# Kernel optimization log

Measured on AMD Instinct MI355X. Metric: run time of the kernel, lower is better.

## Reference

```python
import jax, jax.numpy as jnp
import numpy as np

EPS = 1e-5  # BatchNorm eps (eval mode, running mean 0 / var 1)
NEG_SLOPE = 0.2


def _knn_idx(x, k):
    # x: [B,C,N] -> idx [B,N,k] (indices of k largest of negative sq dist = k nearest)
    inner = jnp.einsum('bcn,bcm->bnm', x, x)
    xx = jnp.sum(x * x, axis=1)  # [B,N]
    pd = 2.0 * inner - xx[:, :, None] - xx[:, None, :]
    return jax.lax.top_k(pd, k)[1]


def _edge_feature(x, k):
    # x: [B,C,N] -> edge features [B,2C,N,k] = concat(neighbor - center, center)
    idx = _knn_idx(x, k)                        # [B,N,k]
    xt = jnp.transpose(x, (0, 2, 1))            # [B,N,C]
    nbr = jax.vmap(lambda f, i: f[i])(xt, idx)  # [B,N,k,C] gather per batch
    ctr = jnp.broadcast_to(xt[:, :, None, :], nbr.shape)
    feat = jnp.concatenate([nbr - ctr, ctr], axis=-1)  # [B,N,k,2C]
    return jnp.transpose(feat, (0, 3, 1, 2))


def _bn(x, g, b):
    # eval-mode BatchNorm: running_mean=0, running_var=1 -> x * g/sqrt(1+eps) + b
    inv = 1.0 / np.sqrt(1.0 + EPS)
    sh = (1, -1) + (1,) * (x.ndim - 2)
    return x * (g * inv).reshape(sh) + b.reshape(sh)


def _lrelu(x):
    return jnp.where(x >= 0, x, NEG_SLOPE * x)


def _conv2d(x, w, b):  # 1x1 Conv2d: x [B,Ci,N,K], w [Ci,Co]
    return jnp.einsum('bcnk,co->bonk', x, w) + b[None, :, None, None]


def _conv1d(x, w, b):  # 1x1 Conv1d: x [B,Ci,N], w [Ci,Co]
    return jnp.einsum('bcn,co->bon', x, w) + b[None, :, None]


def setup_inputs() -> dict:
    key = jax.random.key(0)
    ks = jax.random.split(key, 24)
    B, N = 8, 4096
    rn = lambda k, sh, s=0.1: (jax.random.normal(k, sh, dtype=jnp.float32) * s)
    inp = {
        'point': jax.random.normal(ks[0], (B, 3, N), dtype=jnp.float32),
        # conv1_1: Conv2d(6,64)
        'w11': rn(ks[1], (6, 64)), 'b11': rn(ks[2], (64,)),
        'g11': jnp.ones((64,), jnp.float32), 'bb11': jnp.zeros((64,), jnp.float32),
        # conv1_2: Conv2d(6,64)
        'w12': rn(ks[3], (6, 64)), 'b12': rn(ks[4], (64,)),
        'g12': jnp.ones((64,), jnp.float32), 'bb12': jnp.zeros((64,), jnp.float32),
        # conv1_3: Conv1d(128,64)
        'w13': rn(ks[5], (128, 64)), 'b13': rn(ks[6], (64,)),
        'g13': jnp.ones((64,), jnp.float32), 'bb13': jnp.zeros((64,), jnp.float32),
        # conv1_5: Conv2d(128,64)
        'w15': rn(ks[7], (128, 64)), 'b15': rn(ks[8], (64,)),
        'g15': jnp.ones((64,), jnp.float32), 'bb15': jnp.zeros((64,), jnp.float32),
        # conv1_4: Conv1d(64,128)
        'w14': rn(ks[9], (64, 128)), 'b14': rn(ks[10], (128,)),
        'g14': jnp.ones((128,), jnp.float32), 'bb14': jnp.zeros((128,), jnp.float32),
        # fc1: Linear(128,64) + ReLU + Linear(64,3)
        'wf1': rn(ks[11], (128, 64)), 'bf1': rn(ks[12], (64,)),
        'wf2': rn(ks[13], (64, 3)), 'bf2': rn(ks[14], (3,)),
    }
    return inp


def reference(point, w11, b11, g11, bb11, w12, b12, g12, bb12,
              w13, b13, g13, bb13, w15, b15, g15, bb15,
              w14, b14, g14, bb14, wf1, bf1, wf2, bf2):
    # point: [B,3,N]
    f = _edge_feature(point, 8)                    # [B,6,N,8]
    f1 = _lrelu(_bn(_conv2d(f, w11, b11), g11, bb11)).max(axis=-1)   # [B,64,N]
    f = _edge_feature(point, 16)                   # [B,6,N,16]
    f2 = _lrelu(_bn(_conv2d(f, w12, b12), g12, bb12)).max(axis=-1)   # [B,64,N]
    f = jnp.concatenate([f1, f2], axis=1)          # [B,128,N]
    f = _lrelu(_bn(_conv1d(f, w13, b13), g13, bb13))                 # [B,64,N]
    g = _edge_feature(f, 16)                       # [B,128,N,16]
    g = _lrelu(_bn(_conv2d(g, w15, b15), g15, bb15)).max(axis=-1)    # [B,64,N]
    g = _lrelu(_bn(_conv1d(g, w14, b14), g14, bb14))                 # [B,128,N]
    feat = jnp.transpose(g, (0, 2, 1))             # [B,N,128]
    h = jax.nn.relu(feat @ wf1 + bf1) @ wf2 + bf2  # [B,N,3]
    refinepoint = h + jnp.transpose(point, (0, 2, 1))
    return feat, refinepoint
```

## Files before the change

kernel.cpp:

```cpp
#include <hip/hip_runtime.h>
#include <math.h>

#define NB 8
#define NP 4096
#define FEAT_SZ (NB * NP * 128)
#define INVBN 0.9999950000374999f
#define SPLIT 2
#define CHUNKS 32

typedef unsigned long long u64;
typedef unsigned int u32;

__device__ __forceinline__ u32 fmap(float f) {
    u32 b = __float_as_uint(f);
    return b ^ ((u32)((int)b >> 31) | 0x80000000u);
}

__device__ __forceinline__ u64 umax64(u64 a, u64 b) { return a > b ? a : b; }

__device__ __forceinline__ void kins(u64 (&v)[16], u64 key) {
    if (key <= v[15]) return;
    bool bb[16];
#pragma unroll
    for (int j = 0; j < 16; ++j) bb[j] = key > v[j];
#pragma unroll
    for (int j = 15; j >= 1; --j) v[j] = bb[j] ? (bb[j - 1] ? v[j - 1] : key) : v[j];
    if (bb[0]) v[0] = key;
}

__device__ __forceinline__ void bufpush(u64 (&v)[16], u64 &q0, u64 &q1, u64 &q2, u64 &q3,
                                        int &cnt, u64 key) {
    if (cnt < 4) {
        q0 = cnt == 0 ? key : q0;
        q1 = cnt == 1 ? key : q1;
        q2 = cnt == 2 ? key : q2;
        q3 = cnt == 3 ? key : q3;
        ++cnt;
    } else {
        kins(v, key);
    }
}

__device__ __forceinline__ void bufflush(u64 (&v)[16], u64 &q0, u64 &q1, u64 &q2, u64 &q3,
                                         int &cnt) {
    kins(v, q0); kins(v, q1); kins(v, q2); kins(v, q3);
    q0 = 0; q1 = 0; q2 = 0; q3 = 0; cnt = 0;
}

__device__ __forceinline__ void bclean(u64 (&v)[16]) {
#pragma unroll
    for (int d = 8; d; d >>= 1) {
#pragma unroll
        for (int i = 0; i < 16; ++i) {
            if ((i & d) == 0) {
                u64 a = v[i], b = v[i | d];
                bool s = a < b;
                v[i] = s ? b : a;
                v[i | d] = s ? a : b;
            }
        }
    }
}

__device__ __forceinline__ void merge_shfl(u64 (&v)[16], int off) {
    u64 o[16];
#pragma unroll
    for (int j = 0; j < 16; ++j) o[j] = __shfl_down(v[j], off);
#pragma unroll
    for (int j = 0; j < 16; ++j) {
        u64 b = o[15 - j];
        v[j] = v[j] > b ? v[j] : b;
    }
    bclean(v);
}

__device__ __forceinline__ u64 rowmax8(u64 x) {
    x = umax64(x, __shfl_xor(x, 1));
    x = umax64(x, __shfl_xor(x, 2));
    x = umax64(x, __shfl_xor(x, 4));
    return x;
}

__global__ __launch_bounds__(256) void knn_point_kernel(const float* __restrict__ point,
                                                        int* __restrict__ idxP) {
    __shared__ float4 pts[NP];
    int bt = blockIdx.x >> 7;
    int n0 = (blockIdx.x & 127) << 5;
    const float* pb = point + (size_t)bt * 3 * NP;
    for (int m = threadIdx.x; m < NP; m += 256) {
        float x = pb[m], y = pb[NP + m], z = pb[2 * NP + m];
        pts[m] = make_float4(x, y, z, fmaf(z, z, fmaf(y, y, x * x)));
    }
    __syncthreads();
    int t = threadIdx.x;
    int q = t & 7;
    float4 c = pts[n0 + (t >> 3)];
    u64 v[16];
#pragma unroll
    for (int j = 0; j < 16; ++j) v[j] = 0;
    u64 b0 = 0, b1 = 0, b2 = 0, b3 = 0;
    int cnt = 0;
    u64 th = 0;
#pragma unroll 1
    for (int o = 0; o < 8; ++o) {
#pragma unroll 4
        for (int ii = 0; ii < 64; ++ii) {
            int m = (((o << 6) + ii) << 3) + q;
            float4 p = pts[m];
            float inner = fmaf(c.z, p.z, fmaf(c.y, p.y, c.x * p.x));
            float pd = fmaf(2.0f, inner, -c.w) - p.w;
            u64 key = ((u64)fmap(pd) << 32) | (u64)(u32)~m;
            if (key > th) bufpush(v, b0, b1, b2, b3, cnt, key);
        }
        if (__any(cnt >= 3)) {
            bufflush(v, b0, b1, b2, b3, cnt);
            th = rowmax8(v[15]);
        }
    }
    bufflush(v, b0, b1, b2, b3, cnt);
    merge_shfl(v, 4);
    merge_shfl(v, 2);
    merge_shfl(v, 1);
    if (q == 0) {
        int* op = idxP + ((size_t)bt * NP + n0 + (t >> 3)) * 16;
#pragma unroll
        for (int j = 0; j < 16; ++j) op[j] = (int)~(u32)v[j];
    }
}

__global__ __launch_bounds__(256) void edge12_kernel(
    const float* __restrict__ point, const int* __restrict__ idxP,
    const float* __restrict__ w11, const float* __restrict__ b11,
    const float* __restrict__ g11, const float* __restrict__ bb11,
    const float* __restrict__ w12, const float* __restrict__ b12,
    const float* __restrict__ g12, const float* __restrict__ bb12,
    float* __restrict__ f12) {
    int lane = threadIdx.x & 63;
    int pt = blockIdx.x * 4 + (threadIdx.x >> 6);
    int bt = pt >> 12, n = pt & (NP - 1);
    const float* pb = point + (size_t)bt * 3 * NP;
    float wd1[3], wc1[3], wd2[3], wc2[3];
#pragma unroll
    for (int c = 0; c < 3; ++c) {
        wd1[c] = w11[c * 64 + lane]; wc1[c] = w11[(3 + c) * 64 + lane];
        wd2[c] = w12[c * 64 + lane]; wc2[c] = w12[(3 + c) * 64 + lane];
    }
    float s1 = g11[lane] * INVBN, sh1 = bb11[lane];
    float s2 = g12[lane] * INVBN, sh2 = bb12[lane];
    float cx = pb[n], cy = pb[NP + n], cz = pb[2 * NP + n];
    float base1 = fmaf(wc1[2], cz, fmaf(wc1[1], cy, fmaf(wc1[0], cx, b11[lane])));
    float base2 = fmaf(wc2[2], cz, fmaf(wc2[1], cy, fmaf(wc2[0], cx, b12[lane])));
    float a1 = -INFINITY, a2 = -INFINITY;
    const int* nb = idxP + (size_t)pt * 16;
#pragma unroll
    for (int j = 0; j < 16; ++j) {
        int m = nb[j];
        float ex = pb[m] - cx, ey = pb[NP + m] - cy, ez = pb[2 * NP + m] - cz;
        float y2 = fmaf(wd2[2], ez, fmaf(wd2[1], ey, fmaf(wd2[0], ex, base2)));
        float z2 = fmaf(y2, s2, sh2);
        z2 = z2 >= 0.f ? z2 : 0.2f * z2;
        a2 = fmaxf(a2, z2);
        if (j < 8) {
            float y1 = fmaf(wd1[2], ez, fmaf(wd1[1], ey, fmaf(wd1[0], ex, base1)));
            float z1 = fmaf(y1, s1, sh1);
            z1 = z1 >= 0.f ? z1 : 0.2f * z1;
            a1 = fmaxf(a1, z1);
        }
    }
    f12[((size_t)pt << 7) + lane] = a1;
    f12[((size_t)pt << 7) + 64 + lane] = a2;
}

template<int K, int O, int MODE>
__global__ __launch_bounds__(256) void gemm_act_kernel(
        const float* __restrict__ in, const float* __restrict__ W,
        const float* __restrict__ b, const float* __restrict__ g,
        const float* __restrict__ s, float* __restrict__ outp) {
    __shared__ float A[64 * (K + 1)];
    __shared__ float Wl[K * O];
    constexpr int F4R = K / 4;
#pragma unroll
    for (int i = 0; i < 64 * F4R / 256; ++i) {
        int f = threadIdx.x + i * 256;
        int pt = f / F4R, c4 = f % F4R;
        float4 v = *(const float4*)(in + ((size_t)blockIdx.x * 64 + pt) * K + c4 * 4);
        float* d = A + pt * (K + 1) + c4 * 4;
        d[0] = v.x; d[1] = v.y; d[2] = v.z; d[3] = v.w;
    }
    if constexpr (MODE == 0) {
#pragma unroll
        for (int i = 0; i < 8; ++i) {
            int f = threadIdx.x + i * 256;
            int half = f >= 1024;
            int fr = f & 1023;
            int c = fr >> 4, o4 = fr & 15;
            const float* src = half ? (W + (64 + c) * 64 + o4 * 4) : (W + c * 64 + o4 * 4);
            float4 v = *(const float4*)src;
            float* d = Wl + c * 128 + half * 64 + o4 * 4;
            d[0] = v.x; d[1] = v.y; d[2] = v.z; d[3] = v.w;
        }
    } else {
#pragma unroll
        for (int i = 0; i < K * O / 1024; ++i) {
            int f = threadIdx.x + i * 256;
            *(float4*)(Wl + f * 4) = *(const float4*)(W + f * 4);
        }
    }
    __syncthreads();
    constexpr int NO = O / 8;
    int po = threadIdx.x & 7, pp = threadIdx.x >> 3;
    int pt0 = pp * 2, o0 = po * NO;
    float acc[2][NO];
#pragma unroll
    for (int i = 0; i < NO; ++i) {
        int o = o0 + i;
        float init;
        if constexpr (MODE == 0) init = (o < 64) ? 0.f : b[o - 64];
        else init = b[o];
        acc[0][i] = init;
        acc[1][i] = init;
    }
#pragma unroll 8
    for (int kk = 0; kk < K; ++kk) {
        float a0 = A[pt0 * (K + 1) + kk];
        float a1 = A[(pt0 + 1) * (K + 1) + kk];
        float w[NO];
#pragma unroll
        for (int i4 = 0; i4 < NO / 4; ++i4) {
            float4 wv = *(const float4*)(Wl + kk * O + o0 + i4 * 4);
            w[i4 * 4 + 0] = wv.x; w[i4 * 4 + 1] = wv.y;
            w[i4 * 4 + 2] = wv.z; w[i4 * 4 + 3] = wv.w;
        }
#pragma unroll
        for (int i = 0; i < NO; ++i) {
            acc[0][i] = fmaf(a0, w[i], acc[0][i]);
            acc[1][i] = fmaf(a1, w[i], acc[1][i]);
        }
    }
#pragma unroll
    for (int p = 0; p < 2; ++p) {
        size_t rowg = (size_t)blockIdx.x * 64 + pt0 + p;
#pragma unroll
        for (int i4 = 0; i4 < NO / 4; ++i4) {
            float4 ov;
            float t[4];
#pragma unroll
            for (int j = 0; j < 4; ++j) {
                int o = o0 + i4 * 4 + j;
                float a = acc[p][i4 * 4 + j];
                if constexpr (MODE == 0) {
                    t[j] = a;
                } else if constexpr (MODE == 1) {
                    float vv = fmaf(a, g[o] * INVBN, s[o]);
                    t[j] = vv >= 0.f ? vv : 0.2f * vv;
                } else {
                    t[j] = fmaxf(a, 0.f);
                }
            }
            ov.x = t[0]; ov.y = t[1]; ov.z = t[2]; ov.w = t[3];
            *(float4*)(outp + rowg * O + o0 + i4 * 4) = ov;
        }
    }
}

__global__ __launch_bounds__(256) void xxf_kernel(const float* __restrict__ h1t,
                                                  float* __restrict__ xxf) {
    int lane = threadIdx.x & 63;
    int pt = blockIdx.x * 4 + (threadIdx.x >> 6);
    float h = h1t[((size_t)pt << 6) + lane];
    float s = 0.f;
#pragma unroll
    for (int c = 0; c < 64; ++c) { float hc = __shfl(h, c); s = fmaf(hc, hc, s); }
    if (lane == 0) xxf[pt] = s;
}

__global__ __launch_bounds__(256, 2) void knn_feat_kernel(const float* __restrict__ h1t,
                                                          const float* __restrict__ xxf,
                                                          u64* __restrict__ partF) {
    __shared__ __align__(16) char smem[81920];
    float* At = (float*)smem;
    float* Bt = (float*)(smem + 32768);
    u32*   Sb = (u32*)(smem + 49152);
    int seg = blockIdx.x & 1;
    int rg  = (blockIdx.x >> 1) & 31;
    int bt  = blockIdx.x >> 6;
    int n0  = rg << 7;
    int tid = threadIdx.x;
    int rp = tid >> 4;
    int cg = tid & 15;
    int cs = cg << 2;
    const float* hbase = h1t + ((size_t)bt * NP << 6);
    const float* hA = hbase + ((size_t)n0 << 6);
#pragma unroll
    for (int rep = 0; rep < 8; ++rep) {
        int row = rep * 16 + rp;
        float4 va = *(const float4*)(hA + (row << 6) + cs);
        float fv[4] = {va.x, va.y, va.z, va.w};
#pragma unroll
        for (int i = 0; i < 4; ++i) {
            int ch = cs + i;
            int rw = row ^ ((row & 32) >> 3) ^ (((ch >> 2) & 7) << 2);
            At[ch * 128 + rw] = fv[i];
        }
    }
    int m00 = seg * (CHUNKS * 64);
#pragma unroll
    for (int rep = 0; rep < 4; ++rep) {
        int col = rep * 16 + rp;
        float4 vb = *(const float4*)(hbase + ((size_t)(m00 + col) << 6) + cs);
        float fv[4] = {vb.x, vb.y, vb.z, vb.w};
#pragma unroll
        for (int i = 0; i < 4; ++i) {
            int ch = cs + i;
            int cl = col ^ ((col & 32) >> 3) ^ (((ch >> 2) & 7) << 2);
            Bt[ch * 64 + cl] = fv[i];
        }
    }
    float xa[8];
    {
        const float* xap = xxf + bt * NP + n0 + rp * 8;
        float4 t0 = *(const float4*)xap;
        float4 t1 = *(const float4*)(xap + 4);
        xa[0]=t0.x; xa[1]=t0.y; xa[2]=t0.z; xa[3]=t0.w;
        xa[4]=t1.x; xa[5]=t1.y; xa[6]=t1.z; xa[7]=t1.w;
    }
    int r = tid >> 1, h = tid & 1;
    u64 v[16];
#pragma unroll
    for (int j = 0; j < 16; ++j) v[j] = 0;
    u64 q0 = 0, q1 = 0, q2 = 0, q3 = 0;
    int cnt = 0;
    u32 th32 = 0;
    int ab0 = (rp * 8) ^ (rp & 4);
    int ab1 = (rp * 8 + 4) ^ (rp & 4);
    int cb0 = (cg * 4) ^ ((cg & 8) >> 1);
    int swQ = ((r ^ (r >> 3)) & 7) << 2;
    __syncthreads();
#pragma unroll 1
    for (int mcl = 0; mcl < CHUNKS; ++mcl) {
        int m0c = m00 + (mcl << 6);
        bool more = (mcl + 1) < CHUNKS;
        float4 nv0, nv1, nv2, nv3;
        if (more) {
            const float* hn = hbase + ((size_t)(m0c + 64) << 6);
            nv0 = *(const float4*)(hn + ((0 * 16 + rp) << 6) + cs);
            nv1 = *(const float4*)(hn + ((1 * 16 + rp) << 6) + cs);
            nv2 = *(const float4*)(hn + ((2 * 16 + rp) << 6) + cs);
            nv3 = *(const float4*)(hn + ((3 * 16 + rp) << 6) + cs);
        }
        float4 xbv = *(const float4*)(xxf + bt * NP + m0c + (cg << 2));
        float acc[8][4];
#pragma unroll
        for (int i = 0; i < 8; ++i)
#pragma unroll
            for (int j = 0; j < 4; ++j) acc[i][j] = 0.f;
#pragma unroll 4
        for (int kk = 0; kk < 64; ++kk) {
            int sw = ((kk >> 2) & 7) << 2;
            const float* Ak = At + (kk << 7);
            float4 a0 = *(const float4*)(Ak + (ab0 ^ sw));
            float4 a1 = *(const float4*)(Ak + (ab1 ^ sw));
            float4 bq = *(const float4*)(Bt + (kk << 6) + (cb0 ^ sw));
            float av[8] = {a0.x, a0.y, a0.z, a0.w, a1.x, a1.y, a1.z, a1.w};
            float bv[4] = {bq.x, bq.y, bq.z, bq.w};
#pragma unroll
            for (int i = 0; i < 8; ++i)
#pragma unroll
                for (int j = 0; j < 4; ++j)
                    acc[i][j] = fmaf(av[i], bv[j], acc[i][j]);
        }
        float xbs[4] = {xbv.x, xbv.y, xbv.z, xbv.w};
#pragma unroll
        for (int i = 0; i < 8; ++i) {
            int row = rp * 8 + i;
            u32 k0, k1, k2, k3;
            {
                float pd;
                pd = fmaf(2.0f, acc[i][0], -xa[i]) - xbs[0]; k0 = fmap(pd);
                pd = fmaf(2.0f, acc[i][1], -xa[i]) - xbs[1]; k1 = fmap(pd);
                pd = fmaf(2.0f, acc[i][2], -xa[i]) - xbs[2]; k2 = fmap(pd);
                pd = fmaf(2.0f, acc[i][3], -xa[i]) - xbs[3]; k3 = fmap(pd);
            }
            int sq = ((row ^ (row >> 3)) & 7) << 2;
            *(uint4*)(Sb + row * 64 + ((cg << 2) ^ sq)) = make_uint4(k0, k1, k2, k3);
        }
        __syncthreads();
#pragma unroll
        for (int sI = 0; sI < 8; ++sI) {
            int c0 = h * 32 + (sI << 2);
            uint4 kq = *(const uint4*)(Sb + r * 64 + (c0 ^ swQ));
            u32 m01 = kq.x > kq.y ? kq.x : kq.y;
            u32 m23 = kq.z > kq.w ? kq.z : kq.w;
            u32 mx = m01 > m23 ? m01 : m23;
            if (mx >= th32) {
                u32 ks[4] = {kq.x, kq.y, kq.z, kq.w};
#pragma unroll
                for (int j = 0; j < 4; ++j) {
                    if (ks[j] >= th32) {
                        u64 key = ((u64)ks[j] << 32) | (u64)(u32)~(m0c + c0 + j);
                        bufpush(v, q0, q1, q2, q3, cnt, key);
                    }
                }
            }
        }
        if (more) {
            float fva[4][4] = {{nv0.x, nv0.y, nv0.z, nv0.w}, {nv1.x, nv1.y, nv1.z, nv1.w},
                               {nv2.x, nv2.y, nv2.z, nv2.w}, {nv3.x, nv3.y, nv3.z, nv3.w}};
#pragma unroll
            for (int rep = 0; rep < 4; ++rep) {
                int col = rep * 16 + rp;
#pragma unroll
                for (int i = 0; i < 4; ++i) {
                    int ch = cs + i;
                    int cl = col ^ ((col & 32) >> 3) ^ (((ch >> 2) & 7) << 2);
                    Bt[ch * 64 + cl] = fva[rep][i];
                }
            }
        }
        if (__any(cnt >= 3)) {
            bufflush(v, q0, q1, q2, q3, cnt);
            u64 m = umax64(v[15], __shfl_xor(v[15], 1));
            th32 = (u32)(m >> 32);
        }
        __syncthreads();
    }
    bufflush(v, q0, q1, q2, q3, cnt);
    merge_shfl(v, 1);
    if (h == 0) {
        u64* op = partF + (((size_t)bt * NP + n0 + r) * SPLIT + seg) * 16;
#pragma unroll
        for (int j = 0; j < 16; ++j) op[j] = v[j];
    }
}

__global__ __launch_bounds__(256) void edge5_combine_kernel(const float* __restrict__ ZC,
        const u64* __restrict__ partF,
        const float* __restrict__ g15, const float* __restrict__ bb15,
        float* __restrict__ g64t) {
    __shared__ int midx[4][16];
    int lane = threadIdx.x & 63;
    int w = threadIdx.x >> 6;
    int pt = blockIdx.x * 4 + w;
    int bt = pt >> 12;
    if (lane == 0) {
        const u64* base = partF + (size_t)pt * (SPLIT * 16);
        u64 a[16];
#pragma unroll
        for (int j = 0; j < 16; ++j) a[j] = base[j];
#pragma unroll
        for (int j = 0; j < 16; ++j) {
            u64 x = base[16 + (15 - j)];
            a[j] = a[j] > x ? a[j] : x;
        }
        bclean(a);
#pragma unroll
        for (int j = 0; j < 16; ++j) midx[w][j] = (int)~(u32)a[j];
    }
    __syncthreads();
    const float* zrow = ZC + ((size_t)pt << 7);
    float zn = zrow[lane];
    float d = zrow[64 + lane] - zn;
    float sc = g15[lane] * INVBN, sh = bb15[lane];
    const float* zb = ZC + (((size_t)bt * NP) << 7);
    float a = -INFINITY;
    float zm = zb[((size_t)midx[w][0] << 7) + lane];
#pragma unroll 1
    for (int j = 0; j < 16; ++j) {
        float zc = zm;
        if (j < 15) zm = zb[((size_t)midx[w][j + 1] << 7) + lane];
        float y = zc + d;
        float z = fmaf(y, sc, sh);
        z = z >= 0.f ? z : 0.2f * z;
        a = fmaxf(a, z);
    }
    g64t[((size_t)pt << 6) + lane] = a;
}

__global__ __launch_bounds__(256) void fc2_kernel(const float* __restrict__ rbuf,
        const float* __restrict__ point,
        const float* __restrict__ wf2, const float* __restrict__ bf2,
        float* __restrict__ out) {
    int lane = threadIdx.x & 63;
    int pt = blockIdx.x * 4 + (threadIdx.x >> 6);
    int bt = pt >> 12, n = pt & (NP - 1);
    float r = rbuf[((size_t)pt << 6) + lane];
    float s0 = r * wf2[lane * 3 + 0];
    float s1 = r * wf2[lane * 3 + 1];
    float s2 = r * wf2[lane * 3 + 2];
#pragma unroll
    for (int k = 1; k < 64; k <<= 1) {
        s0 += __shfl_xor(s0, k);
        s1 += __shfl_xor(s1, k);
        s2 += __shfl_xor(s2, k);
    }
    if (lane < 3) {
        float hh = lane == 0 ? s0 : (lane == 1 ? s1 : s2);
        float p = point[((size_t)bt * 3 + lane) * NP + n];
        out[(size_t)FEAT_SZ + (size_t)pt * 3 + lane] = hh + bf2[lane] + p;
    }
}

extern "C" void kernel_launch(void* const* d_in, const int* in_sizes, int n_in,
                              void* d_out, int out_size, void* d_ws, size_t ws_size,
                              hipStream_t stream) {
    (void)in_sizes; (void)n_in; (void)out_size; (void)ws_size;
    const float* point = (const float*)d_in[0];
    const float* w11 = (const float*)d_in[1];
    const float* b11 = (const float*)d_in[2];
    const float* g11 = (const float*)d_in[3];
    const float* bb11 = (const float*)d_in[4];
    const float* w12 = (const float*)d_in[5];
    const float* b12 = (const float*)d_in[6];
    const float* g12 = (const float*)d_in[7];
    const float* bb12 = (const float*)d_in[8];
    const float* w13 = (const float*)d_in[9];
    const float* b13 = (const float*)d_in[10];
    const float* g13 = (const float*)d_in[11];
    const float* bb13 = (const float*)d_in[12];
    const float* w15 = (const float*)d_in[13];
    const float* b15 = (const float*)d_in[14];
    const float* g15 = (const float*)d_in[15];
    const float* bb15 = (const float*)d_in[16];
    const float* w14 = (const float*)d_in[17];
    const float* b14 = (const float*)d_in[18];
    const float* g14 = (const float*)d_in[19];
    const float* bb14 = (const float*)d_in[20];
    const float* wf1 = (const float*)d_in[21];
    const float* bf1 = (const float*)d_in[22];
    const float* wf2 = (const float*)d_in[23];
    const float* bf2 = (const float*)d_in[24];

    char* ws = (char*)d_ws;
    int*   idxP  = (int*)ws;
    float* xxf   = (float*)(ws + (2u << 20));
    float* h1t   = (float*)(ws + (4u << 20));
    float* g64t  = (float*)(ws + (4u << 20));
    u64*   partF = (u64*)(ws + (12u << 20));
    float* rbuf  = (float*)(ws + (12u << 20));
    float* f12   = (float*)(ws + (20u << 20));
    float* ZC    = (float*)(ws + (20u << 20));
    float* feat  = (float*)d_out;

    knn_point_kernel<<<dim3(NB * 128), dim3(256), 0, stream>>>(point, idxP);
    edge12_kernel<<<dim3(NB * NP / 4), dim3(256), 0, stream>>>(
        point, idxP, w11, b11, g11, bb11, w12, b12, g12, bb12, f12);
    gemm_act_kernel<128, 64, 1><<<dim3(NB * NP / 64), dim3(256), 0, stream>>>(
        f12, w13, b13, g13, bb13, h1t);
    xxf_kernel<<<dim3(NB * NP / 4), dim3(256), 0, stream>>>(h1t, xxf);
    knn_feat_kernel<<<dim3(NB * 32 * SPLIT), dim3(256), 0, stream>>>(h1t, xxf, partF);
    gemm_act_kernel<64, 128, 0><<<dim3(NB * NP / 64), dim3(256), 0, stream>>>(
        h1t, w15, b15, nullptr, nullptr, ZC);
    edge5_combine_kernel<<<dim3(NB * NP / 4), dim3(256), 0, stream>>>(
        ZC, partF, g15, bb15, g64t);
    gemm_act_kernel<64, 128, 1><<<dim3(NB * NP / 64), dim3(256), 0, stream>>>(
        g64t, w14, b14, g14, bb14, feat);
    gemm_act_kernel<128, 64, 2><<<dim3(NB * NP / 64), dim3(256), 0, stream>>>(
        feat, wf1, bf1, nullptr, nullptr, rbuf);
    fc2_kernel<<<dim3(NB * NP / 4), dim3(256), 0, stream>>>(
        rbuf, point, wf2, bf2, (float*)d_out);
}
```

Baseline: 1.001 ms.

## Fuse squared-norm into conv GEMM and fc1/fc2 into one head kernel

The separate xxf kernel is removed: the conv1_3 GEMM epilogue now writes its activations to shared memory and computes per-point squared norms there. The fc1 GEMM with ReLU and the fc2 reduction plus residual add are merged into a single fc_head kernel, so the intermediate rbuf never goes to global memory. The knn inner product loop is also restructured into groups of four with precomputed swizzled pointers. These cut two launches and a global round trip, at the cost of extra syncs and shared memory in the fused epilogues.

```diff
diff --git a/kernel.cpp b/kernel.cpp
--- a/kernel.cpp
+++ b/kernel.cpp
@@ -171,13 +171,16 @@
     f12[((size_t)pt << 7) + 64 + lane] = a2;
 }
 
-template<int K, int O, int MODE>
+template<int K, int O, int MODE, bool XX>
 __global__ __launch_bounds__(256) void gemm_act_kernel(
         const float* __restrict__ in, const float* __restrict__ W,
         const float* __restrict__ b, const float* __restrict__ g,
-        const float* __restrict__ s, float* __restrict__ outp) {
-    __shared__ float A[64 * (K + 1)];
-    __shared__ float Wl[K * O];
+        const float* __restrict__ s, float* __restrict__ outp,
+        float* __restrict__ xxo) {
+    __shared__ __align__(16) char smem[64 * (K + 1) * 4 + K * O * 4];
+    float* A  = (float*)smem;
+    float* Wl = (float*)(smem + 64 * (K + 1) * 4);
+    float* Hs = (float*)smem;
     constexpr int F4R = K / 4;
 #pragma unroll
     for (int i = 0; i < 64 * F4R / 256; ++i) {
@@ -237,41 +240,50 @@
             acc[1][i] = fmaf(a1, w[i], acc[1][i]);
         }
     }
+    float tact[2][NO];
+#pragma unroll
+    for (int p = 0; p < 2; ++p) {
+#pragma unroll
+        for (int i = 0; i < NO; ++i) {
+            int o = o0 + i;
+            float a = acc[p][i];
+            if constexpr (MODE == 0) {
+                tact[p][i] = a;
+            } else {
+                float vv = fmaf(a, g[o] * INVBN, s[o]);
+                tact[p][i] = vv >= 0.f ? vv : 0.2f * vv;
+            }
+        }
+    }
 #pragma unroll
     for (int p = 0; p < 2; ++p) {
         size_t rowg = (size_t)blockIdx.x * 64 + pt0 + p;
 #pragma unroll
         for (int i4 = 0; i4 < NO / 4; ++i4) {
             float4 ov;
-            float t[4];
-#pragma unroll
-            for (int j = 0; j < 4; ++j) {
-                int o = o0 + i4 * 4 + j;
-                float a = acc[p][i4 * 4 + j];
-                if constexpr (MODE == 0) {
-                    t[j] = a;
-                } else if constexpr (MODE == 1) {
-                    float vv = fmaf(a, g[o] * INVBN, s[o]);
-                    t[j] = vv >= 0.f ? vv : 0.2f * vv;
-                } else {
-                    t[j] = fmaxf(a, 0.f);
-                }
+            ov.x = tact[p][i4 * 4 + 0]; ov.y = tact[p][i4 * 4 + 1];
+            ov.z = tact[p][i4 * 4 + 2]; ov.w = tact[p][i4 * 4 + 3];
+            *(float4*)(outp + rowg * O + o0 + i4 * 4) = ov;
+        }
+    }
+    if constexpr (XX) {
+        __syncthreads();
+#pragma unroll
+        for (int p = 0; p < 2; ++p)
+#pragma unroll
+            for (int i = 0; i < NO; ++i)
+                Hs[(pt0 + p) * 65 + o0 + i] = tact[p][i];
+        __syncthreads();
+        if (threadIdx.x < 64) {
+            float ss = 0.f;
+#pragma unroll
+            for (int c = 0; c < 64; ++c) {
+                float hc = Hs[threadIdx.x * 65 + c];
+                ss = fmaf(hc, hc, ss);
             }
-            ov.x = t[0]; ov.y = t[1]; ov.z = t[2]; ov.w = t[3];
-            *(float4*)(outp + rowg * O + o0 + i4 * 4) = ov;
-        }
-    }
-}
-
-__global__ __launch_bounds__(256) void xxf_kernel(const float* __restrict__ h1t,
-                                                  float* __restrict__ xxf) {
-    int lane = threadIdx.x & 63;
-    int pt = blockIdx.x * 4 + (threadIdx.x >> 6);
-    float h = h1t[((size_t)pt << 6) + lane];
-    float s = 0.f;
-#pragma unroll
-    for (int c = 0; c < 64; ++c) { float hc = __shfl(h, c); s = fmaf(hc, hc, s); }
-    if (lane == 0) xxf[pt] = s;
+            xxo[(size_t)blockIdx.x * 64 + threadIdx.x] = ss;
+        }
+    }
 }
 
 __global__ __launch_bounds__(256, 2) void knn_feat_kernel(const float* __restrict__ h1t,
@@ -354,20 +366,25 @@
         for (int i = 0; i < 8; ++i)
 #pragma unroll
             for (int j = 0; j < 4; ++j) acc[i][j] = 0.f;
-#pragma unroll 4
-        for (int kk = 0; kk < 64; ++kk) {
-            int sw = ((kk >> 2) & 7) << 2;
-            const float* Ak = At + (kk << 7);
-            float4 a0 = *(const float4*)(Ak + (ab0 ^ sw));
-            float4 a1 = *(const float4*)(Ak + (ab1 ^ sw));
-            float4 bq = *(const float4*)(Bt + (kk << 6) + (cb0 ^ sw));
-            float av[8] = {a0.x, a0.y, a0.z, a0.w, a1.x, a1.y, a1.z, a1.w};
-            float bv[4] = {bq.x, bq.y, bq.z, bq.w};
-#pragma unroll
-            for (int i = 0; i < 8; ++i)
-#pragma unroll
-                for (int j = 0; j < 4; ++j)
-                    acc[i][j] = fmaf(av[i], bv[j], acc[i][j]);
+#pragma unroll 1
+        for (int gI = 0; gI < 16; ++gI) {
+            int sw = (gI & 7) << 2;
+            const float* pa0 = At + (gI << 9) + (ab0 ^ sw);
+            const float* pa1 = At + (gI << 9) + (ab1 ^ sw);
+            const float* pbq = Bt + (gI << 8) + (cb0 ^ sw);
+#pragma unroll
+            for (int u = 0; u < 4; ++u) {
+                float4 a0 = *(const float4*)(pa0 + (u << 7));
+                float4 a1 = *(const float4*)(pa1 + (u << 7));
+                float4 bq = *(const float4*)(pbq + (u << 6));
+                float av[8] = {a0.x, a0.y, a0.z, a0.w, a1.x, a1.y, a1.z, a1.w};
+                float bv[4] = {bq.x, bq.y, bq.z, bq.w};
+#pragma unroll
+                for (int i = 0; i < 8; ++i)
+#pragma unroll
+                    for (int j = 0; j < 4; ++j)
+                        acc[i][j] = fmaf(av[i], bv[j], acc[i][j]);
+            }
         }
         float xbs[4] = {xbv.x, xbv.y, xbv.z, xbv.w};
 #pragma unroll
@@ -476,27 +493,70 @@
     g64t[((size_t)pt << 6) + lane] = a;
 }
 
-__global__ __launch_bounds__(256) void fc2_kernel(const float* __restrict__ rbuf,
+__global__ __launch_bounds__(256) void fc_head_kernel(const float* __restrict__ feat,
         const float* __restrict__ point,
+        const float* __restrict__ wf1, const float* __restrict__ bf1,
         const float* __restrict__ wf2, const float* __restrict__ bf2,
         float* __restrict__ out) {
-    int lane = threadIdx.x & 63;
-    int pt = blockIdx.x * 4 + (threadIdx.x >> 6);
-    int bt = pt >> 12, n = pt & (NP - 1);
-    float r = rbuf[((size_t)pt << 6) + lane];
-    float s0 = r * wf2[lane * 3 + 0];
-    float s1 = r * wf2[lane * 3 + 1];
-    float s2 = r * wf2[lane * 3 + 2];
-#pragma unroll
-    for (int k = 1; k < 64; k <<= 1) {
-        s0 += __shfl_xor(s0, k);
-        s1 += __shfl_xor(s1, k);
-        s2 += __shfl_xor(s2, k);
-    }
-    if (lane < 3) {
-        float hh = lane == 0 ? s0 : (lane == 1 ? s1 : s2);
-        float p = point[((size_t)bt * 3 + lane) * NP + n];
-        out[(size_t)FEAT_SZ + (size_t)pt * 3 + lane] = hh + bf2[lane] + p;
+    __shared__ float A[64 * 129];
+    __shared__ float Wl[128 * 64];
+    __shared__ float wf2l[192];
+    float* R = Wl;
+#pragma unroll
+    for (int i = 0; i < 8; ++i) {
+        int f = threadIdx.x + i * 256;
+        int pt = f >> 5, c4 = f & 31;
+        float4 v = *(const float4*)(feat + ((size_t)blockIdx.x * 64 + pt) * 128 + c4 * 4);
+        float* d = A + pt * 129 + c4 * 4;
+        d[0] = v.x; d[1] = v.y; d[2] = v.z; d[3] = v.w;
+    }
+#pragma unroll
+    for (int i = 0; i < 8; ++i) {
+        int f = threadIdx.x + i * 256;
+        *(float4*)(Wl + f * 4) = *(const float4*)(wf1 + f * 4);
+    }
+    if (threadIdx.x < 48)
+        *(float4*)(wf2l + threadIdx.x * 4) = *(const float4*)(wf2 + threadIdx.x * 4);
+    __syncthreads();
+    int po = threadIdx.x & 7, pp = threadIdx.x >> 3;
+    int pt0 = pp * 2, o0 = po * 8;
+    float acc[2][8];
+#pragma unroll
+    for (int i = 0; i < 8; ++i) { acc[0][i] = bf1[o0 + i]; acc[1][i] = bf1[o0 + i]; }
+#pragma unroll 8
+    for (int kk = 0; kk < 128; ++kk) {
+        float a0 = A[pt0 * 129 + kk];
+        float a1 = A[(pt0 + 1) * 129 + kk];
+        float w[8];
+#pragma unroll
+        for (int i4 = 0; i4 < 2; ++i4) {
+            float4 wv = *(const float4*)(Wl + kk * 64 + o0 + i4 * 4);
+            w[i4 * 4 + 0] = wv.x; w[i4 * 4 + 1] = wv.y;
+            w[i4 * 4 + 2] = wv.z; w[i4 * 4 + 3] = wv.w;
+        }
+#pragma unroll
+        for (int i = 0; i < 8; ++i) {
+            acc[0][i] = fmaf(a0, w[i], acc[0][i]);
+            acc[1][i] = fmaf(a1, w[i], acc[1][i]);
+        }
+    }
+    __syncthreads();
+#pragma unroll
+    for (int p = 0; p < 2; ++p)
+#pragma unroll
+        for (int i = 0; i < 8; ++i)
+            R[(pt0 + p) * 65 + o0 + i] = fmaxf(acc[p][i], 0.f);
+    __syncthreads();
+    if (threadIdx.x < 192) {
+        int pt = threadIdx.x / 3, dim = threadIdx.x - pt * 3;
+        float ssum = 0.f;
+#pragma unroll
+        for (int c = 0; c < 64; ++c)
+            ssum = fmaf(R[pt * 65 + c], wf2l[c * 3 + dim], ssum);
+        int ptg = blockIdx.x * 64 + pt;
+        int bt = ptg >> 12, n = ptg & (NP - 1);
+        float p = point[((size_t)bt * 3 + dim) * NP + n];
+        out[(size_t)FEAT_SZ + (size_t)ptg * 3 + dim] = ssum + bf2[dim] + p;
     }
 }
 
@@ -536,7 +596,6 @@
     float* h1t   = (float*)(ws + (4u << 20));
     float* g64t  = (float*)(ws + (4u << 20));
     u64*   partF = (u64*)(ws + (12u << 20));
-    float* rbuf  = (float*)(ws + (12u << 20));
     float* f12   = (float*)(ws + (20u << 20));
     float* ZC    = (float*)(ws + (20u << 20));
     float* feat  = (float*)d_out;
@@ -544,18 +603,15 @@
     knn_point_kernel<<<dim3(NB * 128), dim3(256), 0, stream>>>(point, idxP);
     edge12_kernel<<<dim3(NB * NP / 4), dim3(256), 0, stream>>>(
         point, idxP, w11, b11, g11, bb11, w12, b12, g12, bb12, f12);
-    gemm_act_kernel<128, 64, 1><<<dim3(NB * NP / 64), dim3(256), 0, stream>>>(
-        f12, w13, b13, g13, bb13, h1t);
-    xxf_kernel<<<dim3(NB * NP / 4), dim3(256), 0, stream>>>(h1t, xxf);
+    gemm_act_kernel<128, 64, 1, true><<<dim3(NB * NP / 64), dim3(256), 0, stream>>>(
+        f12, w13, b13, g13, bb13, h1t, xxf);
     knn_feat_kernel<<<dim3(NB * 32 * SPLIT), dim3(256), 0, stream>>>(h1t, xxf, partF);
-    gemm_act_kernel<64, 128, 0><<<dim3(NB * NP / 64), dim3(256), 0, stream>>>(
-        h1t, w15, b15, nullptr, nullptr, ZC);
+    gemm_act_kernel<64, 128, 0, false><<<dim3(NB * NP / 64), dim3(256), 0, stream>>>(
+        h1t, w15, b15, nullptr, nullptr, ZC, nullptr);
     edge5_combine_kernel<<<dim3(NB * NP / 4), dim3(256), 0, stream>>>(
         ZC, partF, g15, bb15, g64t);
-    gemm_act_kernel<64, 128, 1><<<dim3(NB * NP / 64), dim3(256), 0, stream>>>(
-        g64t, w14, b14, g14, bb14, feat);
-    gemm_act_kernel<128, 64, 2><<<dim3(NB * NP / 64), dim3(256), 0, stream>>>(
-        feat, wf1, bf1, nullptr, nullptr, rbuf);
-    fc2_kernel<<<dim3(NB * NP / 4), dim3(256), 0, stream>>>(
-        rbuf, point, wf2, bf2, (float*)d_out);
-}
+    gemm_act_kernel<64, 128, 1, false><<<dim3(NB * NP / 64), dim3(256), 0, stream>>>(
+        g64t, w14, b14, g14, bb14, feat, nullptr);
+    fc_head_kernel<<<dim3(NB * NP / 64), dim3(256), 0, stream>>>(
+        feat, point, wf1, bf1, wf2, bf2, (float*)d_out);
+}
```

After: 970.6 us. 3.0% less time.
